# Optimization experiments

Hardware: AMD Instinct MI355X
Metric: run time of the kernel (lower is better)

Reference implementation:

```python
import jax, jax.numpy as jnp
import numpy as np

IN_DIM = 1024
HEAD_DIM = 64
NUM_HEADS = 16
SEQ = 4096


def setup_inputs() -> dict:
    key = jax.random.key(0)
    ks = jax.random.split(key, 7)
    s = 1.0 / np.sqrt(IN_DIM)
    return {
        "h": jax.random.normal(ks[0], (SEQ, IN_DIM), dtype=jnp.float32),
        "Wq": jax.random.uniform(ks[1], (IN_DIM, NUM_HEADS * HEAD_DIM), jnp.float32, -s, s),
        "Wk": jax.random.uniform(ks[2], (IN_DIM, NUM_HEADS * HEAD_DIM), jnp.float32, -s, s),
        "Wv": jax.random.uniform(ks[3], (IN_DIM, NUM_HEADS * HEAD_DIM), jnp.float32, -s, s),
        "bq": jax.random.uniform(ks[4], (NUM_HEADS * HEAD_DIM,), jnp.float32, -s, s),
        "bk": jax.random.uniform(ks[5], (NUM_HEADS * HEAD_DIM,), jnp.float32, -s, s),
        "bv": jax.random.uniform(ks[6], (NUM_HEADS * HEAD_DIM,), jnp.float32, -s, s),
    }


def reference(h, Wq, Wk, Wv, bq, bk, bv):
    n = h.shape[0]
    # QKV projections -> [H, S, D]
    q = (h @ Wq + bq).reshape(n, NUM_HEADS, HEAD_DIM).transpose(1, 0, 2)
    k = (h @ Wk + bk).reshape(n, NUM_HEADS, HEAD_DIM).transpose(1, 0, 2)
    v = (h @ Wv + bv).reshape(n, NUM_HEADS, HEAD_DIM).transpose(1, 0, 2)
    scale = 1.0 / np.sqrt(HEAD_DIM).astype(np.float32)
    scores = jnp.einsum('hsd,htd->hst', q, k) * scale  # [H, S, S]
    probs = jax.nn.softmax(scores, axis=-1)
    out = jnp.einsum('hst,htd->hsd', probs, v)  # [H, S, D]
    return out.transpose(1, 0, 2).reshape(n, NUM_HEADS * HEAD_DIM)
```

## Files before the change

kernel.cpp:

```cpp
#include <hip/hip_runtime.h>
#include <hip/hip_bf16.h>

#define IN_DIM    1024
#define HEAD_DIM  64
#define NUM_HEADS 16
#define SEQ       4096

#define QSCALE 0.18033688011112042f

typedef __bf16 bf16;
typedef __attribute__((ext_vector_type(4))) __bf16 bf16x4;
typedef __attribute__((ext_vector_type(8))) __bf16 bf16x8;
typedef __attribute__((ext_vector_type(4))) float floatx4;

__device__ __forceinline__ void async16(bf16* lds, const bf16* g) {
    __builtin_amdgcn_global_load_lds(
        (const __attribute__((address_space(1))) unsigned int*)g,
        (__attribute__((address_space(3))) unsigned int*)lds, 16, 0, 0);
}


__global__ void mha_conv_h(const float* __restrict__ h, bf16* __restrict__ hb) {
    int i = blockIdx.x * blockDim.x + threadIdx.x;
    float4 v = ((const float4*)h)[i];
    bf16x4 r;
    r[0] = (bf16)v.x; r[1] = (bf16)v.y; r[2] = (bf16)v.z; r[3] = (bf16)v.w;
    ((bf16x4*)hb)[i] = r;
}

__global__ void mha_conv_wt(const float* __restrict__ Wq, const float* __restrict__ Wk,
                            const float* __restrict__ Wv, bf16* __restrict__ Wt) {
    __shared__ bf16 tile[64][65];
    const int mat = blockIdx.z;
    const float* W = (mat == 0) ? Wq : (mat == 1) ? Wk : Wv;
    const int k0 = blockIdx.y * 64, n0 = blockIdx.x * 64;
    const int tn = threadIdx.x & 63, tq = threadIdx.x >> 6;
#pragma unroll
    for (int i = 0; i < 16; ++i) {
        int kk = tq + i * 4;
        tile[kk][tn] = (bf16)W[(size_t)(k0 + kk) * 1024 + n0 + tn];
    }
    __syncthreads();
#pragma unroll
    for (int i = 0; i < 16; ++i) {
        int nn = tq + i * 4;
        Wt[((size_t)mat << 20) + (size_t)(n0 + nn) * 1024 + k0 + tn] = tile[tn][nn];
    }
}

__launch_bounds__(256)
__global__ void mha_qkv_gemm(const bf16* __restrict__ hb, const bf16* __restrict__ Wt,
                             const float* __restrict__ bq, const float* __restrict__ bk,
                             const float* __restrict__ bv,
                             bf16* __restrict__ Qb, bf16* __restrict__ Kb,
                             bf16* __restrict__ Vt) {
    __shared__ __align__(16) bf16 As[128 * 32];
    __shared__ __align__(16) bf16 Bs[128 * 32];

    const int lane = threadIdx.x & 63;
    const int wave = threadIdx.x >> 6;
    const int l16  = lane & 15;
    const int quad = lane >> 4;
    const int wm   = wave & 1;
    const int wn   = wave >> 1;

    const int m0  = blockIdx.x * 128;
    const int n0  = blockIdx.y * 128;
    const int mat = n0 >> 10;
    const int nc0 = n0 & 1023;

    const bf16* Wp = Wt + ((size_t)mat << 20);

    floatx4 acc[4][4] = {};
    const int swz = (l16 >> 1) & 3;

    for (int k0 = 0; k0 < IN_DIM; k0 += 32) {
#pragma unroll
        for (int r = 0; r < 2; ++r) {
            int g = wave * 128 + r * 64 + lane;
            int row = g >> 2, c = g & 3;
            int gc = c ^ ((row >> 1) & 3);
            bf16* ldsbase_a = As + (size_t)(wave * 128 + r * 64) * 8;
            bf16* ldsbase_b = Bs + (size_t)(wave * 128 + r * 64) * 8;
            async16(ldsbase_a, hb + (size_t)(m0 + row) * IN_DIM + k0 + gc * 8);
            async16(ldsbase_b, Wp + (size_t)(nc0 + row) * IN_DIM + k0 + gc * 8);
        }
        __syncthreads();

        bf16x8 af[4], bf[4];
#pragma unroll
        for (int mt = 0; mt < 4; ++mt)
            af[mt] = *(const bf16x8*)(As + (size_t)(wm * 64 + mt * 16 + l16) * 32
                                      + ((quad ^ swz) * 8));
#pragma unroll
        for (int nt = 0; nt < 4; ++nt)
            bf[nt] = *(const bf16x8*)(Bs + (size_t)(wn * 64 + nt * 16 + l16) * 32
                                      + ((quad ^ swz) * 8));
#pragma unroll
        for (int mt = 0; mt < 4; ++mt)
#pragma unroll
            for (int nt = 0; nt < 4; ++nt)
                acc[mt][nt] = __builtin_amdgcn_mfma_f32_16x16x32_bf16(af[mt], bf[nt],
                                                                      acc[mt][nt], 0, 0, 0);
        __syncthreads();
    }

    const float* bias = (mat == 0) ? bq : (mat == 1) ? bk : bv;
#pragma unroll
    for (int nt = 0; nt < 4; ++nt) {
        int nc = nc0 + wn * 64 + nt * 16 + l16;
        float bb = bias[nc];
        int head = nc >> 6, d = nc & 63;
#pragma unroll
        for (int mt = 0; mt < 4; ++mt)
#pragma unroll
            for (int r = 0; r < 4; ++r) {
                int srow = m0 + wm * 64 + mt * 16 + quad * 4 + r;
                float v = acc[mt][nt][r] + bb;
                if (mat == 0)
                    Qb[((size_t)head * SEQ + srow) * HEAD_DIM + d] = (bf16)(v * QSCALE);
                else if (mat == 1)
                    Kb[((size_t)head * SEQ + srow) * HEAD_DIM + d] = (bf16)v;
                else
                    Vt[((size_t)head * HEAD_DIM + d) * SEQ + srow] = (bf16)v;
            }
    }
}

__launch_bounds__(512)
__global__ void mha_attn(const bf16* __restrict__ Qb, const bf16* __restrict__ Kb,
                         const bf16* __restrict__ Vt, float* __restrict__ out) {
    __shared__ __align__(16) bf16 Ks[2][64 * 64];
    __shared__ __align__(16) bf16 Vs[2][64 * 64];
    __shared__ __align__(16) bf16 Ps[8][16 * 72];

    const int lane = threadIdx.x & 63;
    const int wave = threadIdx.x >> 6;
    const int l16  = lane & 15;
    const int quad = lane >> 4;

    const int hh    = blockIdx.y;
    const int qbase = blockIdx.x * 128 + wave * 16;

    const bf16* Qh = Qb + (size_t)hh * SEQ * HEAD_DIM;
    const bf16* Kh = Kb + (size_t)hh * SEQ * HEAD_DIM;
    const bf16* Vh = Vt + (size_t)hh * HEAD_DIM * SEQ;

    const int sg   = wave * 64 + lane;
    const int srow = sg >> 3;
    const int sgc  = (sg & 7) ^ (srow & 7);

    bf16x8 qf[2];
#pragma unroll
    for (int ks = 0; ks < 2; ++ks)
        qf[ks] = *(const bf16x8*)(Qh + (size_t)(qbase + l16) * HEAD_DIM + ks * 32 + quad * 8);

    bf16x8 vone;
#pragma unroll
    for (int i = 0; i < 8; ++i) vone[i] = (bf16)1.0f;

    floatx4 o[4] = {};
    floatx4 ol   = {};

    bf16* lp = &Ps[wave][0];
    const int swk = l16 & 7;

    async16(&Ks[0][wave * 512], Kh + (size_t)srow * HEAD_DIM + sgc * 8);
    async16(&Vs[0][wave * 512], Vh + (size_t)srow * SEQ + sgc * 8);
    __syncthreads();

    for (int t0 = 0; t0 < SEQ; t0 += 64) {
        const int cur = (t0 >> 6) & 1, nxt = cur ^ 1;
        if (t0 + 64 < SEQ) {
            async16(&Ks[nxt][wave * 512], Kh + (size_t)(t0 + 64 + srow) * HEAD_DIM + sgc * 8);
            async16(&Vs[nxt][wave * 512], Vh + (size_t)srow * SEQ + t0 + 64 + sgc * 8);
        }

        bf16x8 kf[4][2], vf[4][2];
#pragma unroll
        for (int tt = 0; tt < 4; ++tt)
#pragma unroll
            for (int ks = 0; ks < 2; ++ks)
                kf[tt][ks] = *(const bf16x8*)(&Ks[cur][(size_t)(tt * 16 + l16) * 64
                                              + (((ks * 4 + quad) ^ swk) * 8)]);
#pragma unroll
        for (int dt = 0; dt < 4; ++dt)
#pragma unroll
            for (int ks = 0; ks < 2; ++ks)
                vf[dt][ks] = *(const bf16x8*)(&Vs[cur][(size_t)(dt * 16 + l16) * 64
                                              + (((ks * 4 + quad) ^ swk) * 8)]);

#pragma unroll
        for (int tt = 0; tt < 4; ++tt) {
            floatx4 s = {};
            s = __builtin_amdgcn_mfma_f32_16x16x32_bf16(kf[tt][0], qf[0], s, 0, 0, 0);
            s = __builtin_amdgcn_mfma_f32_16x16x32_bf16(kf[tt][1], qf[1], s, 0, 0, 0);
            bf16x4 pk;
#pragma unroll
            for (int r = 0; r < 4; ++r) pk[r] = (bf16)__builtin_amdgcn_exp2f(s[r]);
            *(bf16x4*)(lp + l16 * 72 + tt * 16 + quad * 4) = pk;
        }

#pragma unroll
        for (int ks = 0; ks < 2; ++ks) {
            bf16x8 pf = *(const bf16x8*)(lp + l16 * 72 + ks * 32 + quad * 8);
#pragma unroll
            for (int dt = 0; dt < 4; ++dt)
                o[dt] = __builtin_amdgcn_mfma_f32_16x16x32_bf16(pf, vf[dt][ks], o[dt], 0, 0, 0);
            ol = __builtin_amdgcn_mfma_f32_16x16x32_bf16(pf, vone, ol, 0, 0, 0);
        }
        __syncthreads();
    }

#pragma unroll
    for (int r = 0; r < 4; ++r) {
        float inv = 1.0f / ol[r];
        int srow_o = qbase + quad * 4 + r;
#pragma unroll
        for (int dt = 0; dt < 4; ++dt)
            out[(size_t)srow_o * (NUM_HEADS * HEAD_DIM) + hh * 64 + dt * 16 + l16]
                = o[dt][r] * inv;
    }
}

extern "C" void kernel_launch(void* const* d_in, const int* in_sizes, int n_in,
                              void* d_out, int out_size, void* d_ws, size_t ws_size,
                              hipStream_t stream) {
    const float* h  = (const float*)d_in[0];
    const float* Wq = (const float*)d_in[1];
    const float* Wk = (const float*)d_in[2];
    const float* Wv = (const float*)d_in[3];
    const float* bq = (const float*)d_in[4];
    const float* bk = (const float*)d_in[5];
    const float* bv = (const float*)d_in[6];
    float* out = (float*)d_out;

    char* ws = (char*)d_ws;
    const size_t MB = 1024 * 1024;
    bf16* hb = (bf16*)(ws);
    bf16* Wt = (bf16*)(ws + 8 * MB);
    bf16* Qb = (bf16*)(ws + 14 * MB);
    bf16* Kb = (bf16*)(ws + 22 * MB);
    bf16* Vt = (bf16*)(ws + 30 * MB);

    mha_conv_h<<<(SEQ * IN_DIM / 4) / 256, 256, 0, stream>>>(h, hb);
    mha_conv_wt<<<dim3(16, 16, 3), 256, 0, stream>>>(Wq, Wk, Wv, Wt);
    mha_qkv_gemm<<<dim3(SEQ / 128, (3 * IN_DIM) / 128), 256, 0, stream>>>(
        hb, Wt, bq, bk, bv, Qb, Kb, Vt);
    mha_attn<<<dim3(SEQ / 128, NUM_HEADS), 512, 0, stream>>>(Qb, Kb, Vt, out);
}
```

Before: 206.5 us.

## Use 32x32x16 MFMA in attention with register-level P transpose

The attention kernel moves from 16x16x32 MFMA tiles to 32x32x16 tiles, so each wave handles 32 query rows and the block shrinks to 256 threads. The LDS round-trip for the probability tile is dropped: exp2 results are packed with v_cvt_pk_bf16_f32 and rearranged across lane halves with v_permlane32_swap so they can feed the PV MFMA directly from registers. This removes the per-tile LDS write and read and raises MFMA work per K/V fragment load. In exchange it uses more accumulator registers and runs fewer waves per block, which may reduce latency hiding.

```diff
diff --git a/kernel.cpp b/kernel.cpp
--- a/kernel.cpp
+++ b/kernel.cpp
@@ -12,11 +12,23 @@
 typedef __attribute__((ext_vector_type(4))) __bf16 bf16x4;
 typedef __attribute__((ext_vector_type(8))) __bf16 bf16x8;
 typedef __attribute__((ext_vector_type(4))) float floatx4;
+typedef __attribute__((ext_vector_type(16))) float floatx16;
+typedef __attribute__((ext_vector_type(4))) unsigned uint32x4;
 
 __device__ __forceinline__ void async16(bf16* lds, const bf16* g) {
     __builtin_amdgcn_global_load_lds(
         (const __attribute__((address_space(1))) unsigned int*)g,
         (__attribute__((address_space(3))) unsigned int*)lds, 16, 0, 0);
+}
+
+__device__ __forceinline__ unsigned cvtpk_bf16(float lo, float hi) {
+    unsigned r;
+    asm("v_cvt_pk_bf16_f32 %0, %1, %2" : "=v"(r) : "v"(lo), "v"(hi));
+    return r;
+}
+
+__device__ __forceinline__ void permswap(unsigned& a, unsigned& b) {
+    asm("v_permlane32_swap_b32 %0, %1" : "+v"(a), "+v"(b));
 }
 
 
@@ -127,99 +139,124 @@
     }
 }
 
-__launch_bounds__(512)
+__launch_bounds__(256)
 __global__ void mha_attn(const bf16* __restrict__ Qb, const bf16* __restrict__ Kb,
                          const bf16* __restrict__ Vt, float* __restrict__ out) {
     __shared__ __align__(16) bf16 Ks[2][64 * 64];
     __shared__ __align__(16) bf16 Vs[2][64 * 64];
-    __shared__ __align__(16) bf16 Ps[8][16 * 72];
 
     const int lane = threadIdx.x & 63;
     const int wave = threadIdx.x >> 6;
-    const int l16  = lane & 15;
-    const int quad = lane >> 4;
-
-    const int hh    = blockIdx.y;
-    const int qbase = blockIdx.x * 128 + wave * 16;
+    const int l31  = lane & 31;
+    const int hi   = lane >> 5;
+
+    const int hh = blockIdx.y;
+    const int q0 = blockIdx.x * 128 + wave * 32;
 
     const bf16* Qh = Qb + (size_t)hh * SEQ * HEAD_DIM;
     const bf16* Kh = Kb + (size_t)hh * SEQ * HEAD_DIM;
     const bf16* Vh = Vt + (size_t)hh * HEAD_DIM * SEQ;
 
-    const int sg   = wave * 64 + lane;
-    const int srow = sg >> 3;
-    const int sgc  = (sg & 7) ^ (srow & 7);
-
-    bf16x8 qf[2];
-#pragma unroll
-    for (int ks = 0; ks < 2; ++ks)
-        qf[ks] = *(const bf16x8*)(Qh + (size_t)(qbase + l16) * HEAD_DIM + ks * 32 + quad * 8);
+    const int sg0   = wave * 64 + lane;
+    const int srow0 = sg0 >> 3;
+    const int sgc   = (sg0 & 7) ^ (srow0 & 7);
+
+    bf16x8 qf[4];
+#pragma unroll
+    for (int ks = 0; ks < 4; ++ks)
+        qf[ks] = *(const bf16x8*)(Qh + (size_t)(q0 + l31) * HEAD_DIM + ks * 16 + hi * 8);
 
     bf16x8 vone;
 #pragma unroll
     for (int i = 0; i < 8; ++i) vone[i] = (bf16)1.0f;
 
-    floatx4 o[4] = {};
-    floatx4 ol   = {};
-
-    bf16* lp = &Ps[wave][0];
-    const int swk = l16 & 7;
-
-    async16(&Ks[0][wave * 512], Kh + (size_t)srow * HEAD_DIM + sgc * 8);
-    async16(&Vs[0][wave * 512], Vh + (size_t)srow * SEQ + sgc * 8);
+    floatx16 o0 = {}, o1 = {}, ol = {};
+    const int swz = l31 & 7;
+
+#pragma unroll
+    for (int r = 0; r < 2; ++r) {
+        async16(&Ks[0][(r * 256 + wave * 64) * 8],
+                Kh + (size_t)(r * 32 + srow0) * HEAD_DIM + sgc * 8);
+        async16(&Vs[0][(r * 256 + wave * 64) * 8],
+                Vh + (size_t)(r * 32 + srow0) * SEQ + sgc * 8);
+    }
     __syncthreads();
 
     for (int t0 = 0; t0 < SEQ; t0 += 64) {
         const int cur = (t0 >> 6) & 1, nxt = cur ^ 1;
         if (t0 + 64 < SEQ) {
-            async16(&Ks[nxt][wave * 512], Kh + (size_t)(t0 + 64 + srow) * HEAD_DIM + sgc * 8);
-            async16(&Vs[nxt][wave * 512], Vh + (size_t)srow * SEQ + t0 + 64 + sgc * 8);
-        }
-
-        bf16x8 kf[4][2], vf[4][2];
-#pragma unroll
-        for (int tt = 0; tt < 4; ++tt)
-#pragma unroll
-            for (int ks = 0; ks < 2; ++ks)
-                kf[tt][ks] = *(const bf16x8*)(&Ks[cur][(size_t)(tt * 16 + l16) * 64
-                                              + (((ks * 4 + quad) ^ swk) * 8)]);
-#pragma unroll
-        for (int dt = 0; dt < 4; ++dt)
-#pragma unroll
-            for (int ks = 0; ks < 2; ++ks)
-                vf[dt][ks] = *(const bf16x8*)(&Vs[cur][(size_t)(dt * 16 + l16) * 64
-                                              + (((ks * 4 + quad) ^ swk) * 8)]);
-
-#pragma unroll
-        for (int tt = 0; tt < 4; ++tt) {
-            floatx4 s = {};
-            s = __builtin_amdgcn_mfma_f32_16x16x32_bf16(kf[tt][0], qf[0], s, 0, 0, 0);
-            s = __builtin_amdgcn_mfma_f32_16x16x32_bf16(kf[tt][1], qf[1], s, 0, 0, 0);
-            bf16x4 pk;
-#pragma unroll
-            for (int r = 0; r < 4; ++r) pk[r] = (bf16)__builtin_amdgcn_exp2f(s[r]);
-            *(bf16x4*)(lp + l16 * 72 + tt * 16 + quad * 4) = pk;
-        }
-
-#pragma unroll
-        for (int ks = 0; ks < 2; ++ks) {
-            bf16x8 pf = *(const bf16x8*)(lp + l16 * 72 + ks * 32 + quad * 8);
-#pragma unroll
-            for (int dt = 0; dt < 4; ++dt)
-                o[dt] = __builtin_amdgcn_mfma_f32_16x16x32_bf16(pf, vf[dt][ks], o[dt], 0, 0, 0);
-            ol = __builtin_amdgcn_mfma_f32_16x16x32_bf16(pf, vone, ol, 0, 0, 0);
+#pragma unroll
+            for (int r = 0; r < 2; ++r) {
+                async16(&Ks[nxt][(r * 256 + wave * 64) * 8],
+                        Kh + (size_t)(t0 + 64 + r * 32 + srow0) * HEAD_DIM + sgc * 8);
+                async16(&Vs[nxt][(r * 256 + wave * 64) * 8],
+                        Vh + (size_t)(r * 32 + srow0) * SEQ + t0 + 64 + sgc * 8);
+            }
+        }
+
+        bf16x8 kf[2][4];
+#pragma unroll
+        for (int tt = 0; tt < 2; ++tt)
+#pragma unroll
+            for (int ks = 0; ks < 4; ++ks)
+                kf[tt][ks] = *(const bf16x8*)(&Ks[cur][(tt * 32 + l31) * 64
+                                              + (((ks * 2 + hi) ^ swz) * 8)]);
+
+        floatx16 s0 = {}, s1 = {};
+#pragma unroll
+        for (int ks = 0; ks < 4; ++ks)
+            s0 = __builtin_amdgcn_mfma_f32_32x32x16_bf16(kf[0][ks], qf[ks], s0, 0, 0, 0);
+#pragma unroll
+        for (int ks = 0; ks < 4; ++ks)
+            s1 = __builtin_amdgcn_mfma_f32_32x32x16_bf16(kf[1][ks], qf[ks], s1, 0, 0, 0);
+
+        bf16x8 vf[2][4];
+#pragma unroll
+        for (int dt = 0; dt < 2; ++dt)
+#pragma unroll
+            for (int sl = 0; sl < 4; ++sl)
+                vf[dt][sl] = *(const bf16x8*)(&Vs[cur][(dt * 32 + l31) * 64
+                                              + (((sl * 2 + hi) ^ swz) * 8)]);
+
+        bf16x8 pa[4];
+#pragma unroll
+        for (int sl = 0; sl < 4; ++sl) {
+            const floatx16 sv = (sl < 2) ? s0 : s1;
+            const int rb = 8 * (sl & 1);
+            float p0 = __builtin_amdgcn_exp2f(sv[rb + 0]);
+            float p1 = __builtin_amdgcn_exp2f(sv[rb + 1]);
+            float p2 = __builtin_amdgcn_exp2f(sv[rb + 2]);
+            float p3 = __builtin_amdgcn_exp2f(sv[rb + 3]);
+            float p4 = __builtin_amdgcn_exp2f(sv[rb + 4]);
+            float p5 = __builtin_amdgcn_exp2f(sv[rb + 5]);
+            float p6 = __builtin_amdgcn_exp2f(sv[rb + 6]);
+            float p7 = __builtin_amdgcn_exp2f(sv[rb + 7]);
+            unsigned u0 = cvtpk_bf16(p0, p1);
+            unsigned u1 = cvtpk_bf16(p2, p3);
+            unsigned u2 = cvtpk_bf16(p4, p5);
+            unsigned u3 = cvtpk_bf16(p6, p7);
+            permswap(u0, u2);
+            permswap(u1, u3);
+            uint32x4 w;
+            w[0] = u0; w[1] = u1; w[2] = u2; w[3] = u3;
+            pa[sl] = __builtin_bit_cast(bf16x8, w);
+        }
+
+#pragma unroll
+        for (int sl = 0; sl < 4; ++sl) {
+            o0 = __builtin_amdgcn_mfma_f32_32x32x16_bf16(pa[sl], vf[0][sl], o0, 0, 0, 0);
+            o1 = __builtin_amdgcn_mfma_f32_32x32x16_bf16(pa[sl], vf[1][sl], o1, 0, 0, 0);
+            ol = __builtin_amdgcn_mfma_f32_32x32x16_bf16(pa[sl], vone, ol, 0, 0, 0);
         }
         __syncthreads();
     }
 
 #pragma unroll
-    for (int r = 0; r < 4; ++r) {
-        float inv = 1.0f / ol[r];
-        int srow_o = qbase + quad * 4 + r;
-#pragma unroll
-        for (int dt = 0; dt < 4; ++dt)
-            out[(size_t)srow_o * (NUM_HEADS * HEAD_DIM) + hh * 64 + dt * 16 + l16]
-                = o[dt][r] * inv;
+    for (int r = 0; r < 16; ++r) {
+        const int q = q0 + (r & 3) + 8 * (r >> 2) + 4 * hi;
+        const float inv = 1.0f / ol[r];
+        out[(size_t)q * (NUM_HEADS * HEAD_DIM) + hh * 64 + l31]      = o0[r] * inv;
+        out[(size_t)q * (NUM_HEADS * HEAD_DIM) + hh * 64 + 32 + l31] = o1[r] * inv;
     }
 }
 
@@ -247,5 +284,5 @@
     mha_conv_wt<<<dim3(16, 16, 3), 256, 0, stream>>>(Wq, Wk, Wv, Wt);
     mha_qkv_gemm<<<dim3(SEQ / 128, (3 * IN_DIM) / 128), 256, 0, stream>>>(
         hb, Wt, bq, bk, bv, Qb, Kb, Vt);
-    mha_attn<<<dim3(SEQ / 128, NUM_HEADS), 512, 0, stream>>>(Qb, Kb, Vt, out);
-}
+    mha_attn<<<dim3(SEQ / 128, NUM_HEADS), 256, 0, stream>>>(Qb, Kb, Vt, out);
+}
```

Result: slower. 211.5 us (+2.4%).
